# Optimization experiments

Hardware: AMD Instinct MI355X
Metric: run time of the kernel (lower is better)

The kernel has to match this reference:

```python
import jax, jax.numpy as jnp
import numpy as np

BS, SL, WPL, NP = 32, 256, 4, 320
WD, PD, RD, HD = 768, 64, 64, 256
PN, RN, PL = 32, 64, 8
NF = 128
WINDOW_SIZES = (2, 3, 4)
FD = 2 * HD  # node feature dim


def setup_inputs() -> dict:
    key = jax.random.key(0)
    ks = jax.random.split(key, 24)
    s = 0.02
    inp = {}
    # forward tensors (bert_out stands in for BertModel output after CLS slice)
    inp["bert_out"] = jax.random.normal(ks[0], (BS, NP, WD), jnp.float32)
    inp["wordpiece_gather_idx"] = jax.random.randint(ks[1], (BS, SL, WPL), 0, NP + 1)
    inp["pos"] = jax.random.randint(ks[2], (BS, SL), 0, PN)
    inp["deprel"] = jax.random.randint(ks[3], (BS, SL), 0, RN)
    inp["path"] = jax.random.randint(ks[4], (BS, SL, PL), 0, 2 * SL + 1)
    inp["aspect_head"] = jax.random.randint(ks[5], (BS, SL), 0, SL + 1)
    inp["text_mask"] = jax.random.randint(ks[6], (BS, SL), 0, 2)
    inp["aspect_mask"] = jax.random.randint(ks[7], (BS, SL), 0, 2)
    # parameters (pad row 0 zeroed to mimic padding_idx)
    inp["pos_emb"] = (jax.random.normal(ks[8], (PN, PD)) * s).at[0].set(0.0)
    inp["deprel_emb"] = (jax.random.normal(ks[9], (RN, RD)) * s).at[0].set(0.0)
    inp["pathdepth_emb"] = (jax.random.normal(ks[10], (PL + 2, PD)) * s).at[0].set(0.0)
    inp["ext_rel"] = jax.random.normal(ks[11], (RD,)) * s
    inp["fc1_W"] = jax.random.normal(ks[12], (WD + 2 * PD, FD)) * s
    inp["fc1_b"] = jnp.zeros((FD,), jnp.float32)
    inp["bilin_W"] = jax.random.normal(ks[13], (2 * FD, RD)) * s
    inp["bilin_b"] = jnp.zeros((), jnp.float32)
    inp["W_k2"] = jax.random.normal(ks[14], (2, FD, NF)) * s
    inp["b_k2"] = jnp.zeros((NF,), jnp.float32)
    inp["W_k3"] = jax.random.normal(ks[15], (3, FD, NF)) * s
    inp["b_k3"] = jnp.zeros((NF,), jnp.float32)
    inp["W_k4"] = jax.random.normal(ks[16], (4, FD, NF)) * s
    inp["b_k4"] = jnp.zeros((NF,), jnp.float32)
    inp["fc_out_W"] = jax.random.normal(ks[17], (NF * 3, 3)) * s
    inp["fc_out_b"] = jnp.zeros((3,), jnp.float32)
    return inp


def reference(bert_out, wordpiece_gather_idx, pos, deprel, path, aspect_head,
              text_mask, aspect_mask, pos_emb, deprel_emb, pathdepth_emb, ext_rel,
              fc1_W, fc1_b, bilin_W, bilin_b,
              W_k2, b_k2, W_k3, b_k3, W_k4, b_k4, fc_out_W, fc_out_b):
    bs, sl = pos.shape
    wd = bert_out.shape[-1]
    fd = fc1_b.shape[0]
    # --- wordpiece -> word averaging (pad piece 0 is a zero vector) ---
    pieces = jnp.concatenate([jnp.zeros((bs, 1, wd), bert_out.dtype), bert_out], axis=1)  # [B, NP+1, WD]
    g = jnp.take_along_axis(pieces, wordpiece_gather_idx.reshape(bs, -1)[..., None], axis=1)
    g = g.reshape(bs, sl, -1, wd)                                   # [B, SL, WPL, WD]
    npieces = (wordpiece_gather_idx != 0).sum(-1, keepdims=True)    # [B, SL, 1]
    word = g.sum(2) / jnp.maximum(npieces, 1).astype(g.dtype)       # [B, SL, WD]
    # --- node features ---
    path_depth = (path != 0).sum(-1)                                # [B, SL]
    node_in = jnp.concatenate([word, pos_emb[pos], pathdepth_emb[path_depth]], -1)
    node = jax.nn.relu(node_in @ fc1_W + fc1_b)                     # [B, SL, FD]
    # --- edge features: gather head nodes (0 = pad word -> zeros) ---
    node_pad = jnp.concatenate([jnp.zeros((bs, 1, fd), node.dtype), node], axis=1)
    dep = jnp.take_along_axis(node_pad, aspect_head[..., None], axis=1)  # [B, SL, FD]
    head_text = jnp.concatenate([dep, node], axis=1)                # [B, 2SL, FD]
    tail_text = jnp.concatenate([node, jnp.zeros_like(node)], axis=1)
    edge = jnp.concatenate([head_text, tail_text], axis=-1)         # [B, 2SL, 2FD]
    label = jnp.concatenate([deprel_emb[deprel],
                             jnp.broadcast_to(ext_rel, (bs, sl, ext_rel.shape[0]))], axis=1)
    # bilinear score: x1^T W x2 + b, single output channel
    score = jax.nn.sigmoid(jnp.einsum('bnd,dr,bnr->bn', edge, bilin_W, label) + bilin_b)
    edge_score = jnp.concatenate([jnp.ones((bs, 1), score.dtype), score], axis=1)  # [B, 2SL+1]
    # --- node weight: product of edge scores along dependency path ---
    nw = jnp.prod(jnp.take_along_axis(edge_score[:, None, :], path, axis=2), -1)   # [B, SL]
    nw = jnp.where((text_mask != 0) & (aspect_mask == 0), nw, jnp.zeros_like(nw))
    weight_norm = nw.sum(-1)                                        # [B]
    # --- manual windowed CNN + max pool ---
    pooled = []
    for W, b in ((W_k2, b_k2), (W_k3, b_k3), (W_k4, b_k4)):
        kw = W.shape[0]
        cn = sl - kw + 1
        w_win = jnp.mean(jnp.stack([nw[:, k:k + cn] for k in range(kw)], -1), -1)  # [B, CN]
        y = sum(jnp.einsum('bnf,fm->bnm', node[:, k:k + cn, :], W[k]) for k in range(kw))
        y = w_win[..., None] * y + b                                # [B, CN, NF]
        pooled.append(y.max(axis=1))                                # [B, NF]
    sentence = jnp.concatenate(pooled, -1)
    predicts = sentence @ fc_out_W + fc_out_b                       # [B, 3]
    return predicts, weight_norm
```

## Files before the change

kernel.cpp:

```cpp
#include <hip/hip_runtime.h>
#include <hip/hip_bf16.h>
#include <math.h>

#define BSZ 32
#define SL 256
#define WPL 4
#define NP 320
#define WD 768
#define PD 64
#define RD 64
#define FD 512
#define PL 8
#define NF 128
#define ES_STRIDE 513
#define MROWS (BSZ * SL)
#define NZ 384
#define KZ 2048

typedef __attribute__((ext_vector_type(8))) short bf16x8;
typedef __attribute__((ext_vector_type(4))) float f32x4;
typedef unsigned short ushort_t;
typedef __attribute__((ext_vector_type(4))) ushort_t u16x4;

__device__ __forceinline__ ushort_t f2bf(float x) {
    __hip_bfloat16 h = __float2bfloat16(x);
    return *reinterpret_cast<ushort_t*>(&h);
}
__device__ __forceinline__ float bf2f(ushort_t u) {
    return __uint_as_float(((unsigned)u) << 16);
}

#define NB_GATHER MROWS
#define B_WW   NB_GATHER
#define NB_WW  384
#define B_TAB  (B_WW + NB_WW)
#define NB_TAB 42
#define B_WZT  (B_TAB + NB_TAB)
#define NB_WZT 576
#define B_PAD  (B_WZT + NB_WZT)
#define NB_PAD 2
#define B_UT   (B_PAD + NB_PAD)
#define NB_UT  258
#define NB_TOTAL (B_UT + NB_UT)

__global__ __launch_bounds__(256) void setup_kernel(
    const float* __restrict__ bert, const int* __restrict__ wgi,
    const int* __restrict__ pos, const int* __restrict__ path,
    const float* __restrict__ pos_emb, const float* __restrict__ pd_emb,
    const float* __restrict__ bilin_W, const float* __restrict__ deprel_emb,
    const float* __restrict__ ext_rel, const float* __restrict__ fc1_W,
    const float* __restrict__ fc1_b,
    const float* __restrict__ W2, const float* __restrict__ W3,
    const float* __restrict__ W4,
    ushort_t* __restrict__ word, int* __restrict__ depth,
    ushort_t* __restrict__ Ww, float* __restrict__ posc, float* __restrict__ pdc,
    ushort_t* __restrict__ WzT, ushort_t* __restrict__ node,
    float* __restrict__ Ut, float* __restrict__ v)
{
    const int tid = threadIdx.x;
    const int blk = blockIdx.x;
    if (blk < NB_GATHER) {
        const int bs = blk;
        const int b = bs >> 8;
        const int* gi = wgi + (size_t)bs * WPL;
        const int i0 = gi[0], i1 = gi[1], i2 = gi[2], i3 = gi[3];
        const int npc = (i0 != 0) + (i1 != 0) + (i2 != 0) + (i3 != 0);
        const float inv = 1.0f / (float)(npc > 1 ? npc : 1);
        if (tid < 192) {
            const float4* r0 = (const float4*)(bert + ((size_t)b * NP + (i0 - 1)) * WD);
            const float4* r1 = (const float4*)(bert + ((size_t)b * NP + (i1 - 1)) * WD);
            const float4* r2 = (const float4*)(bert + ((size_t)b * NP + (i2 - 1)) * WD);
            const float4* r3 = (const float4*)(bert + ((size_t)b * NP + (i3 - 1)) * WD);
            float4 s = make_float4(0.f, 0.f, 0.f, 0.f);
            if (i0) { float4 t = r0[tid]; s.x += t.x; s.y += t.y; s.z += t.z; s.w += t.w; }
            if (i1) { float4 t = r1[tid]; s.x += t.x; s.y += t.y; s.z += t.z; s.w += t.w; }
            if (i2) { float4 t = r2[tid]; s.x += t.x; s.y += t.y; s.z += t.z; s.w += t.w; }
            if (i3) { float4 t = r3[tid]; s.x += t.x; s.y += t.y; s.z += t.z; s.w += t.w; }
            u16x4 o;
            o[0] = f2bf(s.x * inv); o[1] = f2bf(s.y * inv);
            o[2] = f2bf(s.z * inv); o[3] = f2bf(s.w * inv);
            *reinterpret_cast<u16x4*>(&word[(size_t)bs * WD + tid * 4]) = o;
        } else if (tid == 192) {
            const int* pp = path + (size_t)bs * PL;
            int pd = 0;
#pragma unroll
            for (int l = 0; l < PL; ++l) pd += (pp[l] != 0);
            depth[bs] = pd;
        }
        return;
    }
    if (blk < B_TAB) {
        __shared__ float s[32][33];
        const int t = blk - B_WW;
        const int kt = t % 24, nt = t / 24;
#pragma unroll
        for (int i = 0; i < 4; ++i) {
            const int idx = i * 256 + tid;
            const int kk = idx >> 5, nn = idx & 31;
            s[kk][nn] = fc1_W[(size_t)(kt * 32 + kk) * FD + nt * 32 + nn];
        }
        __syncthreads();
#pragma unroll
        for (int i = 0; i < 4; ++i) {
            const int idx = i * 256 + tid;
            const int nn = idx >> 5, kk = idx & 31;
            Ww[(size_t)(nt * 32 + nn) * WD + kt * 32 + kk] = f2bf(s[kk][nn]);
        }
        return;
    }
    if (blk < B_WZT) {
        const int r = blk - B_TAB;
#pragma unroll
        for (int h = 0; h < 2; ++h) {
            const int cc = tid + h * 256;
            if (r < 32) {
                float acc = fc1_b[cc];
#pragma unroll
                for (int j = 0; j < PD; ++j)
                    acc += pos_emb[r * PD + j] * fc1_W[(size_t)(WD + j) * FD + cc];
                posc[(size_t)r * FD + cc] = acc;
            } else {
                const int r2 = r - 32;
                float acc = 0.f;
#pragma unroll
                for (int j = 0; j < PD; ++j)
                    acc += pd_emb[r2 * PD + j] * fc1_W[(size_t)(WD + PD + j) * FD + cc];
                pdc[(size_t)r2 * FD + cc] = acc;
            }
        }
        return;
    }
    if (blk < B_PAD) {
        __shared__ float s[32][33];
        const int t2 = blk - B_WZT;
        const int p = t2 / 64, tt = t2 % 64;
        const int dt = tt & 15, ft = tt >> 4;
        int w, k; const float* src;
        if (p < 2)      { w = 0; k = p;     src = W2; }
        else if (p < 5) { w = 1; k = p - 2; src = W3; }
        else            { w = 2; k = p - 5; src = W4; }
#pragma unroll
        for (int i = 0; i < 4; ++i) {
            const int idx = i * 256 + tid;
            const int dd = idx >> 5, ff = idx & 31;
            s[dd][ff] = src[((size_t)k * FD + dt * 32 + dd) * NF + ft * 32 + ff];
        }
        __syncthreads();
#pragma unroll
        for (int i = 0; i < 4; ++i) {
            const int idx = i * 256 + tid;
            const int ff = idx >> 5, dd = idx & 31;
            WzT[(size_t)(w * NF + ft * 32 + ff) * KZ + k * FD + dt * 32 + dd] = f2bf(s[dd][ff]);
        }
        return;
    }
    if (blk < B_UT) {
        const int local = (blk - B_PAD) * 256 + tid;
#pragma unroll
        for (int j = 0; j < 3; ++j) node[(size_t)MROWS * FD + local * 3 + j] = 0;
        return;
    }
    {
        const int idx = (blk - B_UT) * 256 + tid;
        if (idx < 65536) {
            const int r = idx >> 10, d = idx & 1023;
            float s = 0.f;
#pragma unroll
            for (int j = 0; j < RD; ++j) s += bilin_W[d * RD + j] * deprel_emb[r * RD + j];
            Ut[idx] = s;
        } else if (idx < 65536 + FD) {
            const int d = idx - 65536;
            float s = 0.f;
#pragma unroll
            for (int j = 0; j < RD; ++j) s += bilin_W[d * RD + j] * ext_rel[j];
            v[d] = s;
        }
        return;
    }
}

__global__ __launch_bounds__(128) void gemm_node(
    const ushort_t* __restrict__ A,
    const ushort_t* __restrict__ Bt,
    const int* __restrict__ pos, const int* __restrict__ depth,
    const float* __restrict__ posc, const float* __restrict__ pdc,
    ushort_t* __restrict__ C)
{
    __shared__ ushort_t As[64 * 128];
    __shared__ ushort_t Bs[64 * 128];
    __shared__ int spos[64], sdep[64];
    const int tid = threadIdx.x;
    const int wid = tid >> 6, lane = tid & 63;
    const int orig = (blockIdx.x & 127) * 8 + (blockIdx.x >> 7);
    const int row0 = (orig >> 3) * 64, col0 = (orig & 7) * 64;
    const int lr = lane & 15, lk = lane >> 4;
    if (tid < 64) { spos[tid] = pos[row0 + tid]; sdep[tid] = depth[row0 + tid]; }
    f32x4 acc[2][4] = {};
    const ushort_t* gA0 = A + (size_t)row0 * WD;
    const ushort_t* gB0 = Bt + (size_t)col0 * WD;
    for (int k0 = 0; k0 < WD; k0 += 128) {
#pragma unroll
        for (int i = 0; i < 8; ++i) {
            const int c = i * 128 + tid;
            const int r = c >> 4, q = (c & 15) ^ (r & 15);
            __builtin_amdgcn_global_load_lds(
                (const __attribute__((address_space(1))) void*)(gA0 + (size_t)r * WD + k0 + q * 8),
                (__attribute__((address_space(3))) void*)((char*)As + (size_t)c * 16),
                16, 0, 0);
        }
#pragma unroll
        for (int i = 0; i < 8; ++i) {
            const int c = i * 128 + tid;
            const int r = c >> 4, q = (c & 15) ^ (r & 15);
            __builtin_amdgcn_global_load_lds(
                (const __attribute__((address_space(1))) void*)(gB0 + (size_t)r * WD + k0 + q * 8),
                (__attribute__((address_space(3))) void*)((char*)Bs + (size_t)c * 16),
                16, 0, 0);
        }
        __syncthreads();
#pragma unroll
        for (int ks = 0; ks < 4; ++ks) {
            bf16x8 af[2], bfv[4];
#pragma unroll
            for (int m = 0; m < 2; ++m) {
                const int fr = wid * 32 + m * 16 + lr;
                af[m] = *reinterpret_cast<const bf16x8*>(
                    &As[fr * 128 + ((((ks << 2) | lk) ^ (fr & 15)) << 3)]);
            }
#pragma unroll
            for (int n = 0; n < 4; ++n) {
                const int fr = n * 16 + lr;
                bfv[n] = *reinterpret_cast<const bf16x8*>(
                    &Bs[fr * 128 + ((((ks << 2) | lk) ^ (fr & 15)) << 3)]);
            }
#pragma unroll
            for (int m = 0; m < 2; ++m)
#pragma unroll
                for (int n = 0; n < 4; ++n)
                    acc[m][n] = __builtin_amdgcn_mfma_f32_16x16x32_bf16(
                        af[m], bfv[n], acc[m][n], 0, 0, 0);
        }
        __syncthreads();
    }
#pragma unroll
    for (int n = 0; n < 4; ++n) {
        const int col = col0 + n * 16 + lr;
#pragma unroll
        for (int m = 0; m < 2; ++m) {
            const f32x4 vv = acc[m][n];
#pragma unroll
            for (int j = 0; j < 4; ++j) {
                const int rloc = wid * 32 + m * 16 + lk * 4 + j;
                const float bv = posc[(size_t)spos[rloc] * FD + col]
                               + pdc[(size_t)sdep[rloc] * FD + col];
                C[(size_t)(row0 + rloc) * FD + col] = f2bf(fmaxf(vv[j] + bv, 0.f));
            }
        }
    }
}

__global__ __launch_bounds__(256) void score_kernel(
    const ushort_t* __restrict__ node, const int* __restrict__ aspect_head,
    const int* __restrict__ deprel, const float* __restrict__ Ut,
    const float* __restrict__ v, const float* __restrict__ bilin_b,
    float* __restrict__ edge_score)
{
    const int g = blockIdx.x * 4 + (threadIdx.x >> 6);
    const int lane = threadIdx.x & 63;
    const int b = g >> 9;
    const int n = g & 511;
    const int d0 = lane * 8;
    typedef __attribute__((ext_vector_type(8))) unsigned short u16x8;
    float sum = 0.f;
    if (n < SL) {
        const int dr = deprel[b * SL + n];
        const int h = aspect_head[b * SL + n];
        const float* uc = Ut + (size_t)dr * 1024;
        const u16x8 nv = *reinterpret_cast<const u16x8*>(&node[((size_t)b * SL + n) * FD + d0]);
        if (h != 0) {
            const u16x8 dv = *reinterpret_cast<const u16x8*>(&node[((size_t)b * SL + (h - 1)) * FD + d0]);
#pragma unroll
            for (int i = 0; i < 8; ++i) sum += bf2f(dv[i]) * uc[d0 + i];
        }
#pragma unroll
        for (int i = 0; i < 8; ++i) sum += bf2f(nv[i]) * uc[FD + d0 + i];
    } else {
        const u16x8 nv = *reinterpret_cast<const u16x8*>(&node[((size_t)b * SL + (n - SL)) * FD + d0]);
#pragma unroll
        for (int i = 0; i < 8; ++i) sum += bf2f(nv[i]) * v[d0 + i];
    }
#pragma unroll
    for (int off = 32; off > 0; off >>= 1) sum += __shfl_xor(sum, off, 64);
    if (lane == 0) {
        const float sc = 1.f / (1.f + expf(-(sum + bilin_b[0])));
        edge_score[b * ES_STRIDE + 1 + n] = sc;
        if (n == 0) edge_score[b * ES_STRIDE] = 1.0f;
    }
}

__global__ __launch_bounds__(128) void gemm_z_pool(
    const ushort_t* __restrict__ node,
    const ushort_t* __restrict__ WzT,
    const float* __restrict__ es,
    const int* __restrict__ path, const int* __restrict__ tmask,
    const int* __restrict__ amask,
    const float* __restrict__ b2, const float* __restrict__ b3,
    const float* __restrict__ b4,
    float* __restrict__ pmaxp)
{
    __shared__ ushort_t As[64 * 128];
    __shared__ ushort_t Bs[64 * 128];
    __shared__ float ses[ES_STRIDE];
    __shared__ float snw[68];
    const int tid = threadIdx.x;
    const int wid = tid >> 6, lane = tid & 63;
    const int orig = (blockIdx.x % 96) * 8 + blockIdx.x / 96;
    const int ct = orig % 6, rt = orig / 6;
    const int row0 = rt * 64, col0 = ct * 64;
    const int lr = lane & 15, lk = lane >> 4;
    f32x4 acc[2][4] = {};
    const ushort_t* gA0 = node + (size_t)row0 * FD;
    const ushort_t* gB0 = WzT + (size_t)col0 * KZ;
    const int w = col0 >> 7;
    const int Keff = (w + 2) * 512;
    for (int k0 = 0; k0 < Keff; k0 += 128) {
#pragma unroll
        for (int i = 0; i < 8; ++i) {
            const int c = i * 128 + tid;
            const int r = c >> 4, q = (c & 15) ^ (r & 15);
            __builtin_amdgcn_global_load_lds(
                (const __attribute__((address_space(1))) void*)(gA0 + (size_t)r * FD + k0 + q * 8),
                (__attribute__((address_space(3))) void*)((char*)As + (size_t)c * 16),
                16, 0, 0);
        }
#pragma unroll
        for (int i = 0; i < 8; ++i) {
            const int c = i * 128 + tid;
            const int r = c >> 4, q = (c & 15) ^ (r & 15);
            __builtin_amdgcn_global_load_lds(
                (const __attribute__((address_space(1))) void*)(gB0 + (size_t)r * KZ + k0 + q * 8),
                (__attribute__((address_space(3))) void*)((char*)Bs + (size_t)c * 16),
                16, 0, 0);
        }
        __syncthreads();
#pragma unroll
        for (int ks = 0; ks < 4; ++ks) {
            bf16x8 af[2], bfv[4];
#pragma unroll
            for (int m = 0; m < 2; ++m) {
                const int fr = wid * 32 + m * 16 + lr;
                af[m] = *reinterpret_cast<const bf16x8*>(
                    &As[fr * 128 + ((((ks << 2) | lk) ^ (fr & 15)) << 3)]);
            }
#pragma unroll
            for (int n = 0; n < 4; ++n) {
                const int fr = n * 16 + lr;
                bfv[n] = *reinterpret_cast<const bf16x8*>(
                    &Bs[fr * 128 + ((((ks << 2) | lk) ^ (fr & 15)) << 3)]);
            }
#pragma unroll
            for (int m = 0; m < 2; ++m)
#pragma unroll
                for (int n = 0; n < 4; ++n)
                    acc[m][n] = __builtin_amdgcn_mfma_f32_16x16x32_bf16(
                        af[m], bfv[n], acc[m][n], 0, 0, 0);
        }
        __syncthreads();
    }
    const int bI = row0 >> 8;
    const int nn0 = row0 & 255;
    const float* esb = es + (size_t)bI * ES_STRIDE;
    for (int i = tid; i < ES_STRIDE; i += 128) ses[i] = esb[i];
    __syncthreads();
    for (int i = tid; i < 68; i += 128) {
        const int s = nn0 + i;
        float p = 0.f;
        if (s < SL) {
            const int* pp = path + ((size_t)bI * SL + s) * PL;
            p = 1.f;
#pragma unroll
            for (int l = 0; l < PL; ++l) p *= ses[pp[l]];
            if (!(tmask[bI * SL + s] != 0 && amask[bI * SL + s] == 0)) p = 0.f;
        }
        snw[i] = p;
    }
    __syncthreads();
    const int kw = w + 2;
    const float invk = (w == 0) ? 0.5f : (w == 1) ? (1.f / 3.f) : 0.25f;
    const float* bias = (w == 0) ? b2 : (w == 1) ? b3 : b4;
    const int nmax = SL - kw;
    float cmax[4];
#pragma unroll
    for (int n = 0; n < 4; ++n) {
        const int col = col0 + n * 16 + lr;
        const float bf = bias[col & 127];
        float mx = -INFINITY;
#pragma unroll
        for (int m = 0; m < 2; ++m) {
            const int rbase = wid * 32 + m * 16 + lk * 4;
            const f32x4 vv = acc[m][n];
#pragma unroll
            for (int j = 0; j < 4; ++j) {
                const int rloc = rbase + j;
                if (nn0 + rloc <= nmax) {
                    float ws = 0.f;
                    for (int k = 0; k < kw; ++k) ws += snw[rloc + k];
                    mx = fmaxf(mx, ws * invk * vv[j] + bf);
                }
            }
        }
        mx = fmaxf(mx, __shfl_xor(mx, 16));
        mx = fmaxf(mx, __shfl_xor(mx, 32));
        cmax[n] = mx;
    }
    if (lane < 16) {
#pragma unroll
        for (int n = 0; n < 4; ++n) {
            const int col = col0 + n * 16 + lr;
            pmaxp[((size_t)rt * 2 + wid) * NZ + col] = cmax[n];
        }
    }
}

__global__ __launch_bounds__(384) void finish_kernel(
    const float* __restrict__ pmaxp, const float* __restrict__ es,
    const int* __restrict__ path, const int* __restrict__ tmask,
    const int* __restrict__ amask,
    const float* __restrict__ W, const float* __restrict__ bias,
    float* __restrict__ out)
{
    __shared__ float ses[ES_STRIDE];
    __shared__ float sent[384];
    __shared__ float red[256];
    const int b = blockIdx.x;
    const int t = threadIdx.x;
    const float* esb = es + (size_t)b * ES_STRIDE;
    for (int i = t; i < ES_STRIDE; i += 384) ses[i] = esb[i];
    const float* p = pmaxp + (size_t)b * 8 * NZ + t;
    float mx = -INFINITY;
#pragma unroll
    for (int i = 0; i < 8; ++i) mx = fmaxf(mx, p[(size_t)i * NZ]);
    sent[t] = mx;
    __syncthreads();
    if (t < 256) {
        const int* pp = path + ((size_t)b * SL + t) * PL;
        float pr = 1.f;
#pragma unroll
        for (int l = 0; l < PL; ++l) pr *= ses[pp[l]];
        if (!(tmask[b * SL + t] != 0 && amask[b * SL + t] == 0)) pr = 0.f;
        red[t] = pr;
    }
    __syncthreads();
    for (int off = 128; off > 0; off >>= 1) {
        if (t < off) red[t] += red[t + off];
        __syncthreads();
    }
    if (t == 0) out[96 + b] = red[0];
    if (t < 3) {
        float acc = bias[t];
        for (int i = 0; i < 384; ++i) acc = fmaf(sent[i], W[i * 3 + t], acc);
        out[b * 3 + t] = acc;
    }
}

extern "C" void kernel_launch(void* const* d_in, const int* in_sizes, int n_in,
                              void* d_out, int out_size, void* d_ws, size_t ws_size,
                              hipStream_t stream)
{
    const float* bert      = (const float*)d_in[0];
    const int*   wgi       = (const int*)d_in[1];
    const int*   pos       = (const int*)d_in[2];
    const int*   deprel    = (const int*)d_in[3];
    const int*   path      = (const int*)d_in[4];
    const int*   ahead     = (const int*)d_in[5];
    const int*   tmask     = (const int*)d_in[6];
    const int*   amask     = (const int*)d_in[7];
    const float* pos_emb   = (const float*)d_in[8];
    const float* dre_emb   = (const float*)d_in[9];
    const float* pd_emb    = (const float*)d_in[10];
    const float* ext_rel   = (const float*)d_in[11];
    const float* fc1_W     = (const float*)d_in[12];
    const float* fc1_b     = (const float*)d_in[13];
    const float* bilin_W   = (const float*)d_in[14];
    const float* bilin_b   = (const float*)d_in[15];
    const float* W2        = (const float*)d_in[16];
    const float* b2        = (const float*)d_in[17];
    const float* W3        = (const float*)d_in[18];
    const float* b3        = (const float*)d_in[19];
    const float* W4        = (const float*)d_in[20];
    const float* b4        = (const float*)d_in[21];
    const float* fco_W     = (const float*)d_in[22];
    const float* fco_b     = (const float*)d_in[23];
    float* out = (float*)d_out;

    uint8_t* w = (uint8_t*)d_ws;
    size_t off = 0;
    ushort_t* word = (ushort_t*)(w + off); off += (size_t)MROWS * WD * 2;
    ushort_t* node = (ushort_t*)(w + off); off += (size_t)(MROWS + 3) * FD * 2;
    ushort_t* Ww   = (ushort_t*)(w + off); off += (size_t)FD * WD * 2;
    ushort_t* WzT  = (ushort_t*)(w + off); off += (size_t)NZ * KZ * 2;
    float* Ut    = (float*)(w + off); off += (size_t)64 * 1024 * 4;
    float* vvec  = (float*)(w + off); off += FD * 4;
    float* posc  = (float*)(w + off); off += (size_t)32 * FD * 4;
    float* pdc   = (float*)(w + off); off += (size_t)10 * FD * 4;
    float* es    = (float*)(w + off); off += (size_t)BSZ * ES_STRIDE * 4;
    float* pmaxp = (float*)(w + off); off += (size_t)256 * NZ * 4;
    int*   depth = (int*)(w + off);  off += (size_t)MROWS * 4;

    setup_kernel<<<NB_TOTAL, 256, 0, stream>>>(
        bert, wgi, pos, path, pos_emb, pd_emb,
        bilin_W, dre_emb, ext_rel, fc1_W, fc1_b, W2, W3, W4,
        word, depth, Ww, posc, pdc, WzT, node, Ut, vvec);

    gemm_node<<<1024, 128, 0, stream>>>(
        word, Ww, pos, depth, posc, pdc, node);

    score_kernel<<<(BSZ * 2 * SL) / 4, 256, 0, stream>>>(
        node, ahead, deprel, Ut, vvec, bilin_b, es);

    gemm_z_pool<<<768, 128, 0, stream>>>(
        node, WzT, es, path, tmask, amask, b2, b3, b4, pmaxp);

    finish_kernel<<<BSZ, 384, 0, stream>>>(
        pmaxp, es, path, tmask, amask, fco_W, fco_b, out);
}
```

Baseline: 92.61 us.

## Fuse finish kernel into pooled GEMM via atomic max and last-block reduction

Removes the separate finish kernel. Each pooling GEMM block atomically max-reduces its column maxima into a per-batch sentence buffer using an order-preserving float-to-uint key. A per-batch counter then lets the last arriving block (of 24) compute the node-weight sum and the output projection. This saves one kernel launch and the partial-max buffer round trip, at the cost of global atomics, threadfences and a serial tail in one block per batch. The change also sets wave priority around the MFMA loops in both GEMMs.

```diff
diff --git a/kernel.cpp b/kernel.cpp
--- a/kernel.cpp
+++ b/kernel.cpp
@@ -29,6 +29,14 @@
 __device__ __forceinline__ float bf2f(ushort_t u) {
     return __uint_as_float(((unsigned)u) << 16);
 }
+__device__ __forceinline__ unsigned fkey(float f) {
+    unsigned b = __float_as_uint(f);
+    return (b & 0x80000000u) ? ~b : (b | 0x80000000u);
+}
+__device__ __forceinline__ float funkey(unsigned k) {
+    return (k & 0x80000000u) ? __uint_as_float(k & 0x7FFFFFFFu)
+                             : __uint_as_float(~k);
+}
 
 #define NB_GATHER MROWS
 #define B_WW   NB_GATHER
@@ -41,7 +49,9 @@
 #define NB_PAD 2
 #define B_UT   (B_PAD + NB_PAD)
 #define NB_UT  258
-#define NB_TOTAL (B_UT + NB_UT)
+#define B_Z    (B_UT + NB_UT)
+#define NB_Z   49
+#define NB_TOTAL (B_Z + NB_Z)
 
 __global__ __launch_bounds__(256) void setup_kernel(
     const float* __restrict__ bert, const int* __restrict__ wgi,
@@ -55,7 +65,8 @@
     ushort_t* __restrict__ word, int* __restrict__ depth,
     ushort_t* __restrict__ Ww, float* __restrict__ posc, float* __restrict__ pdc,
     ushort_t* __restrict__ WzT, ushort_t* __restrict__ node,
-    float* __restrict__ Ut, float* __restrict__ v)
+    float* __restrict__ Ut, float* __restrict__ v,
+    unsigned* __restrict__ sentAtom, int* __restrict__ bcount)
 {
     const int tid = threadIdx.x;
     const int blk = blockIdx.x;
@@ -160,7 +171,7 @@
         for (int j = 0; j < 3; ++j) node[(size_t)MROWS * FD + local * 3 + j] = 0;
         return;
     }
-    {
+    if (blk < B_Z) {
         const int idx = (blk - B_UT) * 256 + tid;
         if (idx < 65536) {
             const int r = idx >> 10, d = idx & 1023;
@@ -175,6 +186,12 @@
             for (int j = 0; j < RD; ++j) s += bilin_W[d * RD + j] * ext_rel[j];
             v[d] = s;
         }
+        return;
+    }
+    {
+        const int idx = (blk - B_Z) * 256 + tid;
+        if (idx < BSZ * NZ) sentAtom[idx] = 0u;
+        else if (idx < BSZ * NZ + BSZ) bcount[idx - BSZ * NZ] = 0;
         return;
     }
 }
@@ -218,6 +235,7 @@
                 16, 0, 0);
         }
         __syncthreads();
+        __builtin_amdgcn_s_setprio(1);
 #pragma unroll
         for (int ks = 0; ks < 4; ++ks) {
             bf16x8 af[2], bfv[4];
@@ -240,6 +258,7 @@
                     acc[m][n] = __builtin_amdgcn_mfma_f32_16x16x32_bf16(
                         af[m], bfv[n], acc[m][n], 0, 0, 0);
         }
+        __builtin_amdgcn_s_setprio(0);
         __syncthreads();
     }
 #pragma unroll
@@ -306,12 +325,19 @@
     const int* __restrict__ amask,
     const float* __restrict__ b2, const float* __restrict__ b3,
     const float* __restrict__ b4,
-    float* __restrict__ pmaxp)
+    unsigned* __restrict__ sentAtom,
+    int* __restrict__ bcount,
+    const float* __restrict__ fcoW, const float* __restrict__ fcob,
+    float* __restrict__ out)
 {
     __shared__ ushort_t As[64 * 128];
     __shared__ ushort_t Bs[64 * 128];
     __shared__ float ses[ES_STRIDE];
     __shared__ float snw[68];
+    __shared__ float cshare[2][64];
+    __shared__ float ssent[NZ];
+    __shared__ float red[128];
+    __shared__ int sflag;
     const int tid = threadIdx.x;
     const int wid = tid >> 6, lane = tid & 63;
     const int orig = (blockIdx.x % 96) * 8 + blockIdx.x / 96;
@@ -343,6 +369,7 @@
                 16, 0, 0);
         }
         __syncthreads();
+        __builtin_amdgcn_s_setprio(1);
 #pragma unroll
         for (int ks = 0; ks < 4; ++ks) {
             bf16x8 af[2], bfv[4];
@@ -365,6 +392,7 @@
                     acc[m][n] = __builtin_amdgcn_mfma_f32_16x16x32_bf16(
                         af[m], bfv[n], acc[m][n], 0, 0, 0);
         }
+        __builtin_amdgcn_s_setprio(0);
         __syncthreads();
     }
     const int bI = row0 >> 8;
@@ -389,7 +417,6 @@
     const float invk = (w == 0) ? 0.5f : (w == 1) ? (1.f / 3.f) : 0.25f;
     const float* bias = (w == 0) ? b2 : (w == 1) ? b3 : b4;
     const int nmax = SL - kw;
-    float cmax[4];
 #pragma unroll
     for (int n = 0; n < 4; ++n) {
         const int col = col0 + n * 16 + lr;
@@ -411,55 +438,57 @@
         }
         mx = fmaxf(mx, __shfl_xor(mx, 16));
         mx = fmaxf(mx, __shfl_xor(mx, 32));
-        cmax[n] = mx;
-    }
-    if (lane < 16) {
-#pragma unroll
-        for (int n = 0; n < 4; ++n) {
-            const int col = col0 + n * 16 + lr;
-            pmaxp[((size_t)rt * 2 + wid) * NZ + col] = cmax[n];
-        }
-    }
-}
-
-__global__ __launch_bounds__(384) void finish_kernel(
-    const float* __restrict__ pmaxp, const float* __restrict__ es,
-    const int* __restrict__ path, const int* __restrict__ tmask,
-    const int* __restrict__ amask,
-    const float* __restrict__ W, const float* __restrict__ bias,
-    float* __restrict__ out)
-{
-    __shared__ float ses[ES_STRIDE];
-    __shared__ float sent[384];
-    __shared__ float red[256];
-    const int b = blockIdx.x;
-    const int t = threadIdx.x;
-    const float* esb = es + (size_t)b * ES_STRIDE;
-    for (int i = t; i < ES_STRIDE; i += 384) ses[i] = esb[i];
-    const float* p = pmaxp + (size_t)b * 8 * NZ + t;
-    float mx = -INFINITY;
-#pragma unroll
-    for (int i = 0; i < 8; ++i) mx = fmaxf(mx, p[(size_t)i * NZ]);
-    sent[t] = mx;
+        if (lane < 16) cshare[wid][n * 16 + lr] = mx;
+    }
     __syncthreads();
-    if (t < 256) {
-        const int* pp = path + ((size_t)b * SL + t) * PL;
-        float pr = 1.f;
-#pragma unroll
-        for (int l = 0; l < PL; ++l) pr *= ses[pp[l]];
-        if (!(tmask[b * SL + t] != 0 && amask[b * SL + t] == 0)) pr = 0.f;
-        red[t] = pr;
+    if (tid < 64) {
+        const float f = fmaxf(cshare[0][tid], cshare[1][tid]);
+        atomicMax(&sentAtom[(size_t)bI * NZ + col0 + tid], fkey(f));
     }
     __syncthreads();
-    for (int off = 128; off > 0; off >>= 1) {
-        if (t < off) red[t] += red[t + off];
-        __syncthreads();
-    }
-    if (t == 0) out[96 + b] = red[0];
-    if (t < 3) {
-        float acc = bias[t];
-        for (int i = 0; i < 384; ++i) acc = fmaf(sent[i], W[i * 3 + t], acc);
-        out[b * 3 + t] = acc;
+    if (tid == 0) {
+        __threadfence();
+        sflag = atomicAdd(&bcount[bI], 1);
+    }
+    __syncthreads();
+    if (sflag != 23) return;
+    __threadfence();
+    for (int i = tid; i < NZ; i += 128) {
+        const unsigned k = atomicOr(&sentAtom[(size_t)bI * NZ + i], 0u);
+        ssent[i] = funkey(k);
+    }
+    {
+        float p1 = 0.f, p2 = 0.f;
+        {
+            const int s = tid;
+            const int* pp = path + ((size_t)bI * SL + s) * PL;
+            float p = 1.f;
+#pragma unroll
+            for (int l = 0; l < PL; ++l) p *= ses[pp[l]];
+            if (!(tmask[bI * SL + s] != 0 && amask[bI * SL + s] == 0)) p = 0.f;
+            p1 = p;
+        }
+        {
+            const int s = tid + 128;
+            const int* pp = path + ((size_t)bI * SL + s) * PL;
+            float p = 1.f;
+#pragma unroll
+            for (int l = 0; l < PL; ++l) p *= ses[pp[l]];
+            if (!(tmask[bI * SL + s] != 0 && amask[bI * SL + s] == 0)) p = 0.f;
+            p2 = p;
+        }
+        red[tid] = p1 + p2;
+    }
+    __syncthreads();
+    for (int off = 64; off > 0; off >>= 1) {
+        if (tid < off) red[tid] += red[tid + off];
+        __syncthreads();
+    }
+    if (tid == 0) out[96 + bI] = red[0];
+    if (tid < 3) {
+        float acc2 = fcob[tid];
+        for (int i = 0; i < NZ; ++i) acc2 = fmaf(ssent[i], fcoW[i * 3 + tid], acc2);
+        out[bI * 3 + tid] = acc2;
     }
 }
 
@@ -504,13 +533,15 @@
     float* posc  = (float*)(w + off); off += (size_t)32 * FD * 4;
     float* pdc   = (float*)(w + off); off += (size_t)10 * FD * 4;
     float* es    = (float*)(w + off); off += (size_t)BSZ * ES_STRIDE * 4;
-    float* pmaxp = (float*)(w + off); off += (size_t)256 * NZ * 4;
+    unsigned* sentAtom = (unsigned*)(w + off); off += (size_t)BSZ * NZ * 4;
+    int*   bcount = (int*)(w + off); off += (size_t)BSZ * 4;
     int*   depth = (int*)(w + off);  off += (size_t)MROWS * 4;
 
     setup_kernel<<<NB_TOTAL, 256, 0, stream>>>(
         bert, wgi, pos, path, pos_emb, pd_emb,
         bilin_W, dre_emb, ext_rel, fc1_W, fc1_b, W2, W3, W4,
-        word, depth, Ww, posc, pdc, WzT, node, Ut, vvec);
+        word, depth, Ww, posc, pdc, WzT, node, Ut, vvec,
+        sentAtom, bcount);
 
     gemm_node<<<1024, 128, 0, stream>>>(
         word, Ww, pos, depth, posc, pdc, node);
@@ -519,8 +550,6 @@
         node, ahead, deprel, Ut, vvec, bilin_b, es);
 
     gemm_z_pool<<<768, 128, 0, stream>>>(
-        node, WzT, es, path, tmask, amask, b2, b3, b4, pmaxp);
-
-    finish_kernel<<<BSZ, 384, 0, stream>>>(
-        pmaxp, es, path, tmask, amask, fco_W, fco_b, out);
-}
+        node, WzT, es, path, tmask, amask, b2, b3, b4,
+        sentAtom, bcount, fco_W, fco_b, out);
+}
```

New measurement: 97.78 us. 1.06x slower.
